# Performance work log

Hardware: AMD Instinct MI355X
Metric: run time of the kernel (lower is better)

The kernel has to match this reference:

```python
import jax, jax.numpy as jnp
import numpy as np
from jax import lax

COUNT_NORM_FACTOR = 0.1


def setup_inputs() -> dict:
    key = jax.random.key(0)
    ks = jax.random.split(key, 8)
    B, NA, NT, D = 4096, 16, 16, 128
    task_embeds = jax.random.normal(ks[0], (B, NT, D), dtype=jnp.float32)
    task_nonag_counts = jax.random.uniform(ks[1], (B, NT), dtype=jnp.float32)
    agent_embeds = jax.random.normal(ks[2], (B, NA, D), dtype=jnp.float32)
    task_mask = jnp.zeros((B, NT), dtype=bool)
    agent_mask = jnp.zeros((B, NA), dtype=jnp.float32)  # 0 = active agent
    u = jax.random.uniform(ks[3], (NA, B, NT), dtype=jnp.float32,
                           minval=1e-6, maxval=1.0 - 1e-6)
    gumbels = -jnp.log(-jnp.log(u))
    W_count = jax.random.normal(ks[4], (2, D), dtype=jnp.float32) / np.sqrt(2.0)
    b_count = jnp.zeros((D,), dtype=jnp.float32)
    W_upd = jax.random.normal(ks[5], (2 * D, D), dtype=jnp.float32) / np.sqrt(2.0 * D)
    b_upd = jnp.zeros((D,), dtype=jnp.float32)
    return dict(task_embeds=task_embeds, task_nonag_counts=task_nonag_counts,
                agent_embeds=agent_embeds, task_mask=task_mask,
                agent_mask=agent_mask, gumbels=gumbels,
                W_count=W_count, b_count=b_count, W_upd=W_upd, b_upd=b_upd)


def _autoreg(task_embeds, task_nonag_counts, agent_embeds, task_mask,
             agent_mask, gumbels, W_count, b_count, W_upd, b_upd):
    B, NT, D = task_embeds.shape
    scale = jnp.sqrt(jnp.asarray(D, task_embeds.dtype))
    neg_min = jnp.finfo(task_embeds.dtype).min

    def step(carry, xs):
        te, counts = carry  # te: [B,NT,D], counts: [B,NT]
        ag_emb, g, amask = xs  # [B,D], [B,NT], [B]
        # count embedding: Linear(2, D) on stack([nonag, ag], -1)
        cnt_in = jnp.stack([task_nonag_counts, counts], axis=-1)  # [B,NT,2]
        cnt_e = cnt_in @ W_count + b_count  # [B,NT,D]
        # pointer logits
        logits = jnp.einsum('bd,btd->bt', ag_emb, te + cnt_e) / scale
        masked = jnp.where(task_mask, neg_min, logits)
        # RelaxedOneHotCategorical(temp=1).rsample via gumbel-softmax
        soft = jax.nn.softmax(masked + g, axis=-1)
        onehot = jax.nn.one_hot(jnp.argmax(soft, axis=-1), NT, dtype=soft.dtype)
        hard = onehot - lax.stop_gradient(soft) + soft
        agm = (1.0 - amask)[:, None]  # [B,1]
        hard = hard * agm
        hstop = lax.stop_gradient(hard)
        counts = counts + hstop * COUNT_NORM_FACTOR
        # embedding update: Linear(2D, D) on relu(concat([te, agent_embed]))
        upd_in = jnp.concatenate(
            [te, jnp.broadcast_to(ag_emb[:, None, :], (B, NT, D))], axis=-1)
        upd = jax.nn.relu(upd_in) @ W_upd + b_upd  # [B,NT,D]
        te = te + upd * hstop[..., None] * agm[..., None]
        return (te, counts), hard

    init = (task_embeds, jnp.zeros((B, NT), task_embeds.dtype))
    xs = (jnp.swapaxes(agent_embeds, 0, 1), gumbels, jnp.swapaxes(agent_mask, 0, 1))
    _, allocs = lax.scan(step, init, xs)  # [NA,B,NT]
    return jnp.swapaxes(allocs, 0, 1)  # [B,NA,NT]


def reference(task_embeds, task_nonag_counts, agent_embeds, task_mask,
              agent_mask, gumbels, W_count, b_count, W_upd, b_upd):
    return _autoreg(task_embeds, task_nonag_counts, agent_embeds, task_mask,
                    agent_mask, gumbels, W_count, b_count, W_upd, b_upd)
```

## Files before the change

kernel.cpp:

```cpp
#include <hip/hip_runtime.h>
#include <float.h>
#include <math.h>

#define NBATCH   4096
#define NAGENT   16
#define NTASK    16
#define DDIM     128
#define G        8
#define NTHREADS 512
#define SSEG     20

typedef float f32x2 __attribute__((ext_vector_type(2)));

template<int CTRL>
__device__ __forceinline__ float dppf(float x) {
    return __int_as_float(__builtin_amdgcn_update_dpp(
        0, __float_as_int(x), CTRL, 0xF, 0xF, true));
}
template<int CTRL>
__device__ __forceinline__ int dppi(int x) {
    return __builtin_amdgcn_update_dpp(0, x, CTRL, 0xF, 0xF, true);
}

template<int SEL>
__device__ __forceinline__ void pk_fma_b(f32x2& acc, f32x2 a, f32x2 b) {
    if constexpr (SEL == 0)
        asm("v_pk_fma_f32 %0, %1, %2, %0 op_sel:[0,0,0] op_sel_hi:[0,1,1]"
            : "+v"(acc) : "v"(a), "v"(b));
    else
        asm("v_pk_fma_f32 %0, %1, %2, %0 op_sel:[1,0,0] op_sel_hi:[1,1,1]"
            : "+v"(acc) : "v"(a), "v"(b));
}

template<int CTRL>
__device__ __forceinline__ float merge_dpp(float lo, float hi, bool h) {
    const float a = lo + dppf<CTRL>(lo);
    const float b = hi + dppf<CTRL>(hi);
    return h ? b : a;
}

__global__ void wperm_kernel(const float* __restrict__ W_upd,
                             float4* __restrict__ wp) {
    const int q    = blockIdx.x * 256 + threadIdx.x;
    const int t    = q & 511;
    const int rowc = q >> 9;
    const int i    = (t & 15) * 16 + rowc;
    const int col  = (t >> 4) * 4;
    wp[q] = *(const float4*)(W_upd + (size_t)i * DDIM + col);
}

template<bool PERM>
__global__ __launch_bounds__(NTHREADS)
__attribute__((amdgpu_waves_per_eu(4, 8)))
void alloc_policy_kernel(const float* __restrict__ task_embeds,
                         const float* __restrict__ task_nonag,
                         const float* __restrict__ agent_embeds,
                         const unsigned char* __restrict__ task_mask,
                         const float* __restrict__ agent_mask,
                         const float* __restrict__ gumbels,
                         const float* __restrict__ W_count,
                         const float* __restrict__ b_count,
                         const float* __restrict__ W_upd,
                         const float* __restrict__ b_upd,
                         const float4* __restrict__ wperm,
                         float* __restrict__ out)
{
    __shared__ __align__(16) float te[G][NTASK][DDIM];
    __shared__ __align__(16) float scr[G][16 * SSEG];
    __shared__ __align__(16) float4 sdots4[G][NAGENT];
    __shared__ __align__(16) float4 upd4[G];

    const int tid  = threadIdx.x;
    const int lane = tid & 63;
    const int w    = tid >> 6;
    const int b0   = blockIdx.x * G;
    const int gb_w = b0 + w;

    const bool h0 = (lane & 1) != 0;
    const bool h1 = (lane & 2) != 0;
    const bool h2 = (lane & 4) != 0;
    const bool h3 = (lane & 8) != 0;

    const int cg   = tid >> 4;
    const int iseg = tid & 15;
    const float bu = b_upd[cg * 4 + (tid & 3)];

    const float scalef = sqrtf(128.0f);

    {
        const float4* src = (const float4*)(task_embeds + (size_t)b0 * NTASK * DDIM);
        float4* dst = (float4*)(&te[0][0][0]);
        #pragma unroll
        for (int k = 0; k < (G * NTASK * DDIM / 4) / NTHREADS; ++k)
            dst[k * NTHREADS + tid] = src[k * NTHREADS + tid];
    }

    {
        const int p = tid >> 2, q = tid & 3;
        const int g = p >> 4,  a = p & 15;
        const float* agp = agent_embeds + ((size_t)(b0 + g) * NAGENT + a) * DDIM + q * 32;
        float a0 = 0.f, a1 = 0.f, a2 = 0.f;
        #pragma unroll
        for (int c = 0; c < 8; ++c) {
            const float4 av = *(const float4*)(agp + c * 4);
            const float4 w0 = *(const float4*)(W_count + q * 32 + c * 4);
            const float4 w1 = *(const float4*)(W_count + DDIM + q * 32 + c * 4);
            const float4 bc = *(const float4*)(b_count + q * 32 + c * 4);
            a0 = fmaf(av.x, w0.x, a0); a0 = fmaf(av.y, w0.y, a0);
            a0 = fmaf(av.z, w0.z, a0); a0 = fmaf(av.w, w0.w, a0);
            a1 = fmaf(av.x, w1.x, a1); a1 = fmaf(av.y, w1.y, a1);
            a1 = fmaf(av.z, w1.z, a1); a1 = fmaf(av.w, w1.w, a1);
            a2 = fmaf(av.x, bc.x, a2); a2 = fmaf(av.y, bc.y, a2);
            a2 = fmaf(av.z, bc.z, a2); a2 = fmaf(av.w, bc.w, a2);
        }
        a0 += __shfl_xor(a0, 1); a0 += __shfl_xor(a0, 2);
        a1 += __shfl_xor(a1, 1); a1 += __shfl_xor(a1, 2);
        a2 += __shfl_xor(a2, 1); a2 += __shfl_xor(a2, 2);
        if (q == 0) sdots4[g][a] = make_float4(a0, a1, a2, 0.f);
    }

    const int tau = lane & 15;
    const float nn_my = task_nonag[gb_w * NTASK + tau];
    const unsigned char mask_my = task_mask[gb_w * NTASK + tau];
    float cc_my = 0.0f;

    const float* agbase = agent_embeds + (size_t)gb_w * NAGENT * DDIM;
    float2 ag2 = *(const float2*)(agbase + lane * 2);
    float  gum = gumbels[(size_t)gb_w * NTASK + tau];
    float  amk = agent_mask[(size_t)gb_w * NAGENT + 0];

    __syncthreads();

    for (int a = 0; a < NAGENT; ++a) {
        float v[16];
        #pragma unroll
        for (int t = 0; t < 16; ++t) {
            const float2 t2 = *(const float2*)(&te[w][t][lane * 2]);
            v[t] = fmaf(ag2.y, t2.y, ag2.x * t2.x);
        }
        float p8[8];
        #pragma unroll
        for (int m2 = 0; m2 < 8; ++m2)
            p8[m2] = merge_dpp<0xB1>(v[2 * m2], v[2 * m2 + 1], h0);
        float p4[4];
        #pragma unroll
        for (int m2 = 0; m2 < 4; ++m2)
            p4[m2] = merge_dpp<0x4E>(p8[2 * m2], p8[2 * m2 + 1], h1);
        float p2v[2];
        #pragma unroll
        for (int m2 = 0; m2 < 2; ++m2) {
            const float lo = p4[2 * m2], hi = p4[2 * m2 + 1];
            const float send = h2 ? lo : hi;
            const float mine = h2 ? hi : lo;
            p2v[m2] = mine + __shfl_xor(send, 4);
        }
        float p1;
        {
            const float lo = p2v[0], hi = p2v[1];
            const float send = h3 ? lo : hi;
            const float mine = h3 ? hi : lo;
            p1 = mine + __shfl_xor(send, 8);
        }
        p1 += __shfl_xor(p1, 16);
        p1 += __shfl_xor(p1, 32);

        const float4 sd = sdots4[w][a];
        const float dot_total = p1 + fmaf(nn_my, sd.x, fmaf(cc_my, sd.y, sd.z));
        float z = dot_total / scalef;
        if (mask_my) z = -FLT_MAX;
        z = z + gum;

        float mz = z;
        mz = fmaxf(mz, dppf<0xB1>(mz));
        mz = fmaxf(mz, dppf<0x4E>(mz));
        mz = fmaxf(mz, __shfl_xor(mz, 4));
        mz = fmaxf(mz, __shfl_xor(mz, 8));
        const float e = expf(z - mz);
        float ss = e;
        ss += dppf<0xB1>(ss);
        ss += dppf<0x4E>(ss);
        ss += __shfl_xor(ss, 4);
        ss += __shfl_xor(ss, 8);
        const float sft = e / ss;

        float mx = sft;
        mx = fmaxf(mx, dppf<0xB1>(mx));
        mx = fmaxf(mx, dppf<0x4E>(mx));
        mx = fmaxf(mx, __shfl_xor(mx, 4));
        mx = fmaxf(mx, __shfl_xor(mx, 8));
        int cand = (sft == mx) ? tau : NTASK;
        cand = min(cand, dppi<0xB1>(cand));
        cand = min(cand, dppi<0x4E>(cand));
        cand = min(cand, __shfl_xor(cand, 4));
        cand = min(cand, __shfl_xor(cand, 8));
        const int bi = cand;

        const float agm = 1.0f - amk;
        const float onehot = (tau == bi) ? 1.0f : 0.0f;
        const float hh = ((onehot - sft) + sft) * agm;

        if (lane < 16)
            out[((size_t)gb_w * NAGENT + a) * NTASK + tau] = hh;
        cc_my = cc_my + hh * 0.1f;
        if (lane < 16 && tau == bi)
            upd4[w] = make_float4(__int_as_float(bi), hh, agm, 0.f);

        {
            const float2 tsel = *(const float2*)(&te[w][bi][lane * 2]);
            float2 r0, r1;
            r0.x = fmaxf(tsel.x, 0.f); r0.y = fmaxf(tsel.y, 0.f);
            r1.x = fmaxf(ag2.x, 0.f);  r1.y = fmaxf(ag2.y, 0.f);
            const int i0 = 2 * lane;
            const int i1 = 128 + 2 * lane;
            *(float2*)(&scr[w][(i0 >> 4) * SSEG + (i0 & 15)]) = r0;
            *(float2*)(&scr[w][(i1 >> 4) * SSEG + (i1 & 15)]) = r1;
        }

        const int an = (a + 1) & 15;
        const float2 ag2n = *(const float2*)(agbase + (size_t)an * DDIM + lane * 2);
        const float  gumn = gumbels[((size_t)an * NBATCH + gb_w) * NTASK + tau];
        const float  amkn = agent_mask[(size_t)gb_w * NAGENT + an];

        __syncthreads();

        f32x2 acc01[G], acc23[G];
        #pragma unroll
        for (int g = 0; g < G; ++g) { acc01[g] = f32x2{0.f, 0.f}; acc23[g] = f32x2{0.f, 0.f}; }
        #pragma unroll
        for (int c = 0; c < 4; ++c) {
            float4 Wc0, Wc1, Wc2, Wc3;
            if (PERM) {
                const float4* wp = wperm + (size_t)(c * 4) * 512 + tid;
                Wc0 = wp[0 * 512];
                Wc1 = wp[1 * 512];
                Wc2 = wp[2 * 512];
                Wc3 = wp[3 * 512];
            } else {
                const float* wrow = W_upd + (size_t)(iseg * 16 + c * 4) * DDIM + cg * 4;
                Wc0 = *(const float4*)(wrow + 0 * DDIM);
                Wc1 = *(const float4*)(wrow + 1 * DDIM);
                Wc2 = *(const float4*)(wrow + 2 * DDIM);
                Wc3 = *(const float4*)(wrow + 3 * DDIM);
            }
            const f32x2 w01_0 = f32x2{Wc0.x, Wc0.y}, w23_0 = f32x2{Wc0.z, Wc0.w};
            const f32x2 w01_1 = f32x2{Wc1.x, Wc1.y}, w23_1 = f32x2{Wc1.z, Wc1.w};
            const f32x2 w01_2 = f32x2{Wc2.x, Wc2.y}, w23_2 = f32x2{Wc2.z, Wc2.w};
            const f32x2 w01_3 = f32x2{Wc3.x, Wc3.y}, w23_3 = f32x2{Wc3.z, Wc3.w};
            const int sb = iseg * SSEG + c * 4;
            #pragma unroll
            for (int g = 0; g < 8; ++g) {
                const float4 in4 = *(const float4*)(&scr[g][sb]);
                const f32x2 ixy = f32x2{in4.x, in4.y};
                const f32x2 izw = f32x2{in4.z, in4.w};
                pk_fma_b<0>(acc01[g], ixy, w01_0);
                pk_fma_b<1>(acc01[g], ixy, w01_1);
                pk_fma_b<0>(acc01[g], izw, w01_2);
                pk_fma_b<1>(acc01[g], izw, w01_3);
                pk_fma_b<0>(acc23[g], ixy, w23_0);
                pk_fma_b<1>(acc23[g], ixy, w23_1);
                pk_fma_b<0>(acc23[g], izw, w23_2);
                pk_fma_b<1>(acc23[g], izw, w23_3);
            }
        }
        float q16[16];
        #pragma unroll
        for (int m2 = 0; m2 < 16; ++m2) {
            const float lo = (m2 & 1) ? acc23[m2 >> 1].x : acc01[m2 >> 1].x;
            const float hi = (m2 & 1) ? acc23[m2 >> 1].y : acc01[m2 >> 1].y;
            q16[m2] = merge_dpp<0xB1>(lo, hi, h0);
        }
        float q8[8];
        #pragma unroll
        for (int m2 = 0; m2 < 8; ++m2)
            q8[m2] = merge_dpp<0x4E>(q16[2 * m2], q16[2 * m2 + 1], h1);
        float q4[4];
        #pragma unroll
        for (int m2 = 0; m2 < 4; ++m2) {
            const float lo = q8[2 * m2], hi = q8[2 * m2 + 1];
            const float send = h2 ? lo : hi;
            const float mine = h2 ? hi : lo;
            q4[m2] = mine + __shfl_xor(send, 4);
        }
        float q2[2];
        #pragma unroll
        for (int m2 = 0; m2 < 2; ++m2) {
            const float lo = q4[2 * m2], hi = q4[2 * m2 + 1];
            const float send = h3 ? lo : hi;
            const float mine = h3 ? hi : lo;
            q2[m2] = mine + __shfl_xor(send, 8);
        }
        #pragma unroll
        for (int hgi = 0; hgi < 2; ++hgi) {
            const int g = ((lane & 15) >> 2) + hgi * 4;
            const float4 u4 = upd4[g];
            const int ts = __float_as_int(u4.x);
            const float u = q2[hgi] + bu;
            const float addv = (u * u4.y) * u4.z;
            te[g][ts][cg * 4 + (tid & 3)] += addv;
        }
        __syncthreads();

        ag2 = ag2n; gum = gumn; amk = amkn;
    }
}

extern "C" void kernel_launch(void* const* d_in, const int* in_sizes, int n_in,
                              void* d_out, int out_size, void* d_ws, size_t ws_size,
                              hipStream_t stream) {
    const float*         task_embeds  = (const float*)d_in[0];
    const float*         task_nonag   = (const float*)d_in[1];
    const float*         agent_embeds = (const float*)d_in[2];
    const unsigned char* task_mask    = (const unsigned char*)d_in[3];
    const float*         agent_mask   = (const float*)d_in[4];
    const float*         gumbels      = (const float*)d_in[5];
    const float*         W_count      = (const float*)d_in[6];
    const float*         b_count      = (const float*)d_in[7];
    const float*         W_upd        = (const float*)d_in[8];
    const float*         b_upd        = (const float*)d_in[9];
    float* out = (float*)d_out;

    dim3 grid(NBATCH / G);
    dim3 block(NTHREADS);

    if (ws_size >= 2 * DDIM * DDIM * sizeof(float)) {
        float4* wp = (float4*)d_ws;
        hipLaunchKernelGGL(wperm_kernel, dim3(32), dim3(256), 0, stream, W_upd, wp);
        hipLaunchKernelGGL(alloc_policy_kernel<true>, grid, block, 0, stream,
                           task_embeds, task_nonag, agent_embeds, task_mask,
                           agent_mask, gumbels, W_count, b_count, W_upd, b_upd,
                           wp, out);
    } else {
        hipLaunchKernelGGL(alloc_policy_kernel<false>, grid, block, 0, stream,
                           task_embeds, task_nonag, agent_embeds, task_mask,
                           agent_mask, gumbels, W_count, b_count, W_upd, b_upd,
                           (const float4*)nullptr, out);
    }
}
```

Measured before the change: 111.7 us.

## Retile update GEMV to 8 columns x 4 batches per thread and use DPP row reductions

The update matmul is retiled so each half of the block handles 4 batch groups and each thread covers 8 output columns instead of 4. This halves the scratch loads per thread, doubles reuse of each loaded input, and changes the permuted weight layout and the write-back indexing to match. The softmax and argmax reductions replace the xor-4 and xor-8 shuffles with DPP row_shr/row-mirror style controls so they stay in registers. The DPP controls 0x141 and 0x140 (row half-mirror and row mirror) are not xor permutations, but every lane still ends up with the full 16-lane result. A dummy zero-initialisation loop was also added.

After: 232.9 us. 109% more time.

```diff
diff --git a/kernel.cpp b/kernel.cpp
--- a/kernel.cpp
+++ b/kernel.cpp
@@ -41,11 +41,14 @@
 
 __global__ void wperm_kernel(const float* __restrict__ W_upd,
                              float4* __restrict__ wp) {
-    const int q    = blockIdx.x * 256 + threadIdx.x;
-    const int t    = q & 511;
-    const int rowc = q >> 9;
-    const int i    = (t & 15) * 16 + rowc;
-    const int col  = (t >> 4) * 4;
+    const int q  = blockIdx.x * 256 + threadIdx.x;
+    const int t  = q & 255;
+    const int rh = q >> 8;
+    const int hc = rh & 1;
+    const int di = (rh >> 1) & 3;
+    const int c  = rh >> 3;
+    const int i  = (t & 15) * 16 + c * 4 + di;
+    const int col = (t >> 4) * 8 + hc * 4;
     wp[q] = *(const float4*)(W_upd + (size_t)i * DDIM + col);
 }
 
@@ -81,9 +84,11 @@
     const bool h2 = (lane & 4) != 0;
     const bool h3 = (lane & 8) != 0;
 
-    const int cg   = tid >> 4;
-    const int iseg = tid & 15;
-    const float bu = b_upd[cg * 4 + (tid & 3)];
+    const int halfid = tid >> 8;
+    const int htid   = tid & 255;
+    const int iseg   = htid & 15;
+    const int cg8    = htid >> 4;
+    const float bu = b_upd[cg8 * 8 + (lane & 7)];
 
     const float scalef = sqrtf(128.0f);
 
@@ -149,6 +154,11 @@
         float p2v[2];
         #pragma unroll
         for (int m2 = 0; m2 < 2; ++m2) {
+            const float lo = p2v[m2] = 0.f, hi = 0.f;
+            (void)lo; (void)hi;
+        }
+        #pragma unroll
+        for (int m2 = 0; m2 < 2; ++m2) {
             const float lo = p4[2 * m2], hi = p4[2 * m2 + 1];
             const float send = h2 ? lo : hi;
             const float mine = h2 ? hi : lo;
@@ -173,26 +183,26 @@
         float mz = z;
         mz = fmaxf(mz, dppf<0xB1>(mz));
         mz = fmaxf(mz, dppf<0x4E>(mz));
-        mz = fmaxf(mz, __shfl_xor(mz, 4));
-        mz = fmaxf(mz, __shfl_xor(mz, 8));
+        mz = fmaxf(mz, dppf<0x141>(mz));
+        mz = fmaxf(mz, dppf<0x140>(mz));
         const float e = expf(z - mz);
         float ss = e;
         ss += dppf<0xB1>(ss);
         ss += dppf<0x4E>(ss);
-        ss += __shfl_xor(ss, 4);
-        ss += __shfl_xor(ss, 8);
+        ss += dppf<0x141>(ss);
+        ss += dppf<0x140>(ss);
         const float sft = e / ss;
 
         float mx = sft;
         mx = fmaxf(mx, dppf<0xB1>(mx));
         mx = fmaxf(mx, dppf<0x4E>(mx));
-        mx = fmaxf(mx, __shfl_xor(mx, 4));
-        mx = fmaxf(mx, __shfl_xor(mx, 8));
+        mx = fmaxf(mx, dppf<0x141>(mx));
+        mx = fmaxf(mx, dppf<0x140>(mx));
         int cand = (sft == mx) ? tau : NTASK;
         cand = min(cand, dppi<0xB1>(cand));
         cand = min(cand, dppi<0x4E>(cand));
-        cand = min(cand, __shfl_xor(cand, 4));
-        cand = min(cand, __shfl_xor(cand, 8));
+        cand = min(cand, dppi<0x141>(cand));
+        cand = min(cand, dppi<0x140>(cand));
         const int bi = cand;
 
         const float agm = 1.0f - amk;
@@ -223,52 +233,58 @@
 
         __syncthreads();
 
-        f32x2 acc01[G], acc23[G];
-        #pragma unroll
-        for (int g = 0; g < G; ++g) { acc01[g] = f32x2{0.f, 0.f}; acc23[g] = f32x2{0.f, 0.f}; }
+        f32x2 accP[16];
+        #pragma unroll
+        for (int j = 0; j < 16; ++j) accP[j] = f32x2{0.f, 0.f};
         #pragma unroll
         for (int c = 0; c < 4; ++c) {
-            float4 Wc0, Wc1, Wc2, Wc3;
-            if (PERM) {
-                const float4* wp = wperm + (size_t)(c * 4) * 512 + tid;
-                Wc0 = wp[0 * 512];
-                Wc1 = wp[1 * 512];
-                Wc2 = wp[2 * 512];
-                Wc3 = wp[3 * 512];
-            } else {
-                const float* wrow = W_upd + (size_t)(iseg * 16 + c * 4) * DDIM + cg * 4;
-                Wc0 = *(const float4*)(wrow + 0 * DDIM);
-                Wc1 = *(const float4*)(wrow + 1 * DDIM);
-                Wc2 = *(const float4*)(wrow + 2 * DDIM);
-                Wc3 = *(const float4*)(wrow + 3 * DDIM);
+            const int sb = iseg * SSEG + c * 4;
+            float4 in4[4];
+            #pragma unroll
+            for (int g = 0; g < 4; ++g)
+                in4[g] = *(const float4*)(&scr[halfid * 4 + g][sb]);
+            #pragma unroll
+            for (int hc = 0; hc < 2; ++hc) {
+                float4 W0, W1, W2, W3;
+                if (PERM) {
+                    const float4* wp = wperm + (size_t)(c * 8 + hc) * 256 + htid;
+                    W0 = wp[0 * 256];
+                    W1 = wp[2 * 256];
+                    W2 = wp[4 * 256];
+                    W3 = wp[6 * 256];
+                } else {
+                    const float* wrow = W_upd +
+                        (size_t)(iseg * 16 + c * 4) * DDIM + cg8 * 8 + hc * 4;
+                    W0 = *(const float4*)(wrow + 0 * DDIM);
+                    W1 = *(const float4*)(wrow + 1 * DDIM);
+                    W2 = *(const float4*)(wrow + 2 * DDIM);
+                    W3 = *(const float4*)(wrow + 3 * DDIM);
+                }
+                const f32x2 wA0 = f32x2{W0.x, W0.y}, wB0 = f32x2{W0.z, W0.w};
+                const f32x2 wA1 = f32x2{W1.x, W1.y}, wB1 = f32x2{W1.z, W1.w};
+                const f32x2 wA2 = f32x2{W2.x, W2.y}, wB2 = f32x2{W2.z, W2.w};
+                const f32x2 wA3 = f32x2{W3.x, W3.y}, wB3 = f32x2{W3.z, W3.w};
+                #pragma unroll
+                for (int g = 0; g < 4; ++g) {
+                    const f32x2 ixy = f32x2{in4[g].x, in4[g].y};
+                    const f32x2 izw = f32x2{in4[g].z, in4[g].w};
+                    f32x2& aA = accP[g * 4 + hc * 2];
+                    f32x2& aB = accP[g * 4 + hc * 2 + 1];
+                    pk_fma_b<0>(aA, ixy, wA0);
+                    pk_fma_b<1>(aA, ixy, wA1);
+                    pk_fma_b<0>(aA, izw, wA2);
+                    pk_fma_b<1>(aA, izw, wA3);
+                    pk_fma_b<0>(aB, ixy, wB0);
+                    pk_fma_b<1>(aB, ixy, wB1);
+                    pk_fma_b<0>(aB, izw, wB2);
+                    pk_fma_b<1>(aB, izw, wB3);
+                }
             }
-            const f32x2 w01_0 = f32x2{Wc0.x, Wc0.y}, w23_0 = f32x2{Wc0.z, Wc0.w};
-            const f32x2 w01_1 = f32x2{Wc1.x, Wc1.y}, w23_1 = f32x2{Wc1.z, Wc1.w};
-            const f32x2 w01_2 = f32x2{Wc2.x, Wc2.y}, w23_2 = f32x2{Wc2.z, Wc2.w};
-            const f32x2 w01_3 = f32x2{Wc3.x, Wc3.y}, w23_3 = f32x2{Wc3.z, Wc3.w};
-            const int sb = iseg * SSEG + c * 4;
-            #pragma unroll
-            for (int g = 0; g < 8; ++g) {
-                const float4 in4 = *(const float4*)(&scr[g][sb]);
-                const f32x2 ixy = f32x2{in4.x, in4.y};
-                const f32x2 izw = f32x2{in4.z, in4.w};
-                pk_fma_b<0>(acc01[g], ixy, w01_0);
-                pk_fma_b<1>(acc01[g], ixy, w01_1);
-                pk_fma_b<0>(acc01[g], izw, w01_2);
-                pk_fma_b<1>(acc01[g], izw, w01_3);
-                pk_fma_b<0>(acc23[g], ixy, w23_0);
-                pk_fma_b<1>(acc23[g], ixy, w23_1);
-                pk_fma_b<0>(acc23[g], izw, w23_2);
-                pk_fma_b<1>(acc23[g], izw, w23_3);
-            }
         }
         float q16[16];
         #pragma unroll
-        for (int m2 = 0; m2 < 16; ++m2) {
-            const float lo = (m2 & 1) ? acc23[m2 >> 1].x : acc01[m2 >> 1].x;
-            const float hi = (m2 & 1) ? acc23[m2 >> 1].y : acc01[m2 >> 1].y;
-            q16[m2] = merge_dpp<0xB1>(lo, hi, h0);
-        }
+        for (int m2 = 0; m2 < 16; ++m2)
+            q16[m2] = merge_dpp<0xB1>(accP[m2].x, accP[m2].y, h0);
         float q8[8];
         #pragma unroll
         for (int m2 = 0; m2 < 8; ++m2)
@@ -291,12 +307,12 @@
         }
         #pragma unroll
         for (int hgi = 0; hgi < 2; ++hgi) {
-            const int g = ((lane & 15) >> 2) + hgi * 4;
+            const int g = ((lane >> 3) & 1) + 2 * hgi + 4 * halfid;
             const float4 u4 = upd4[g];
             const int ts = __float_as_int(u4.x);
             const float u = q2[hgi] + bu;
             const float addv = (u * u4.y) * u4.z;
-            te[g][ts][cg * 4 + (tid & 3)] += addv;
+            te[g][ts][cg8 * 8 + (lane & 7)] += addv;
         }
         __syncthreads();
 
```
